# Kernel tuning notes

Measured on AMD Instinct MI355X. Metric: run time of the kernel, lower is better.

Reference implementation:

```python
import jax, jax.numpy as jnp
from jax import lax
import numpy as np

KSIZE = 5  # kernel_size from init
CHANNEL = 256

def _gaussian_kernel2d(sigma, ksize):
    # matches torch: exp(-i^2/(2*sigma^2)) outer product, normalized to sum 1
    n = ksize // 2
    r = jnp.arange(-n, n + 1, dtype=jnp.float32)
    g = jnp.exp(-(r ** 2) / (2.0 * sigma ** 2))
    k2d = g[:, None] * g[None, :]
    return k2d / k2d.sum()

def setup_inputs() -> dict:
    key = jax.random.key(0)
    k1, k2 = jax.random.split(key)
    x = jax.random.normal(k1, (16, CHANNEL, 64, 64), dtype=jnp.float32)
    # sigma is the module's learned scalar; keep away from 0 for a well-defined kernel
    sigma = jax.random.uniform(k2, (1,), dtype=jnp.float32, minval=0.5, maxval=1.5)
    return {"x": x, "sigma": sigma}

def reference(x, sigma):
    # The torch module writes a channel-diagonal weight into a dense Conv2d;
    # mathematically this is a depthwise conv with the same 2D Gaussian per channel.
    C = x.shape[1]
    k2d = _gaussian_kernel2d(sigma[0], KSIZE)
    w = jnp.broadcast_to(k2d[None, None, :, :], (C, 1, KSIZE, KSIZE))  # OIHW, groups=C
    pad = KSIZE // 2
    return lax.conv_general_dilated(
        x, w,
        window_strides=(1, 1),
        padding=[(pad, pad), (pad, pad)],
        dimension_numbers=("NCHW", "OIHW", "NCHW"),
        feature_group_count=C,
    )
```

## Files before the change

kernel.cpp:

```cpp
#include <hip/hip_runtime.h>
#include <math.h>


constexpr int Hh   = 64;
constexpr int Ww   = 64;
constexpr int KS   = 5;
constexpr int PADc = 2;
constexpr int TH   = Hh + 2 * PADc;
constexpr int IN_STR = 72;
constexpr int PPB  = 4;

__global__ __launch_bounds__(256, 4) void gauss5(const float* __restrict__ x,
                                                 const float* __restrict__ sigma,
                                                 float* __restrict__ out) {
    __shared__ alignas(16) float sIn[2][TH * IN_STR];

    const int t = threadIdx.x;
    const size_t plane0 = (size_t)blockIdx.x * PPB;

    const float sg = sigma[0];
    const float c2 = -1.0f / (2.0f * sg * sg);
    float g[KS];
    float gsum = 0.0f;
#pragma unroll
    for (int i = 0; i < KS; ++i) {
        float d = (float)(i - PADc);
        g[i] = expf(d * d * c2);
        gsum += g[i];
    }
    const float ginv = 1.0f / gsum;
#pragma unroll
    for (int i = 0; i < KS; ++i) g[i] *= ginv;

    for (int i = t; i < 528; i += 256) {
        int row, col;
        if (i < 272) {
            int rr = i / 68;
            col = i - rr * 68;
            row = (rr < 2) ? rr : (rr + 64);
        } else {
            int j = i - 272;
            row = 2 + (j >> 2);
            int k = j & 3;
            col = (k < 2) ? k : (k + 64);
        }
        sIn[0][row * IN_STR + col] = 0.0f;
        sIn[1][row * IN_STR + col] = 0.0f;
    }

    const int c4 = t & 15;
    const int r0 = (t >> 4) << 2;

    float4 v[4];
    {
        const float4* __restrict__ x4 = (const float4*)(x + plane0 * (Hh * Ww));
#pragma unroll
        for (int k = 0; k < 4; ++k) v[k] = x4[t + k * 256];
#pragma unroll
        for (int k = 0; k < 4; ++k) {
            int idx = t + k * 256;
            int r   = idx >> 4;
            int c   = (idx & 15) << 2;
            float* dst = &sIn[0][(r + PADc) * IN_STR + c + PADc];
            dst[0] = v[k].x; dst[1] = v[k].y; dst[2] = v[k].z; dst[3] = v[k].w;
        }
    }
    __syncthreads();

    for (int p = 0; p < PPB; ++p) {
        if (p + 1 < PPB) {
            const float4* __restrict__ xn =
                (const float4*)(x + (plane0 + p + 1) * (Hh * Ww));
#pragma unroll
            for (int k = 0; k < 4; ++k) v[k] = xn[t + k * 256];
        }

        const float* __restrict__ buf = sIn[p & 1];
        float4 h[8];
#pragma unroll
        for (int i = 0; i < 8; ++i) {
            const float* src = &buf[(r0 + i) * IN_STR + (c4 << 2)];
            float4 a = *(const float4*)(src);
            float4 b = *(const float4*)(src + 4);
            h[i].x = g[0]*a.x + g[1]*a.y + g[2]*a.z + g[3]*a.w + g[4]*b.x;
            h[i].y = g[0]*a.y + g[1]*a.z + g[2]*a.w + g[3]*b.x + g[4]*b.y;
            h[i].z = g[0]*a.z + g[1]*a.w + g[2]*b.x + g[3]*b.y + g[4]*b.z;
            h[i].w = g[0]*a.w + g[1]*b.x + g[2]*b.y + g[3]*b.z + g[4]*b.w;
        }

        float4* __restrict__ o4 = (float4*)(out + (plane0 + p) * (Hh * Ww));
#pragma unroll
        for (int i = 0; i < 4; ++i) {
            float4 acc;
            acc.x = g[0]*h[i].x; acc.y = g[0]*h[i].y;
            acc.z = g[0]*h[i].z; acc.w = g[0]*h[i].w;
#pragma unroll
            for (int j = 1; j < KS; ++j) {
                acc.x += g[j] * h[i+j].x;
                acc.y += g[j] * h[i+j].y;
                acc.z += g[j] * h[i+j].z;
                acc.w += g[j] * h[i+j].w;
            }
            o4[(r0 + i) * 16 + c4] = acc;
        }

        if (p + 1 < PPB) {
            float* __restrict__ nbuf = sIn[(p + 1) & 1];
#pragma unroll
            for (int k = 0; k < 4; ++k) {
                int idx = t + k * 256;
                int r   = idx >> 4;
                int c   = (idx & 15) << 2;
                float* dst = &nbuf[(r + PADc) * IN_STR + c + PADc];
                dst[0] = v[k].x; dst[1] = v[k].y; dst[2] = v[k].z; dst[3] = v[k].w;
            }
            __syncthreads();
        }
    }
}

extern "C" void kernel_launch(void* const* d_in, const int* in_sizes, int n_in,
                              void* d_out, int out_size, void* d_ws, size_t ws_size,
                              hipStream_t stream) {
    const float* x     = (const float*)d_in[0];
    const float* sigma = (const float*)d_in[1];
    float* out         = (float*)d_out;
    const int planes = in_sizes[0] / (Hh * Ww);
    gauss5<<<planes / PPB, 256, 0, stream>>>(x, sigma, out);
}
```

Baseline: 112.7 us.

## Drop shared-memory staging and read halo directly from global memory per plane

Removes the double-buffered LDS tile and its zero-padded halo. Each thread now loads its 8 input rows straight from global memory, using float4 center loads plus float2 left/right halo loads, and applies masks for the borders. The grid changes from one block per four planes to one block per plane, which gives more blocks and removes the __syncthreads barriers. In exchange, neighbouring threads read overlapping rows redundantly and must rely on L1/L2 to absorb the roughly twofold extra load traffic, and the explicit prefetch overlap is lost.

```diff
diff --git a/kernel.cpp b/kernel.cpp
--- a/kernel.cpp
+++ b/kernel.cpp
@@ -6,17 +6,13 @@
 constexpr int Ww   = 64;
 constexpr int KS   = 5;
 constexpr int PADc = 2;
-constexpr int TH   = Hh + 2 * PADc;
-constexpr int IN_STR = 72;
-constexpr int PPB  = 4;
 
 __global__ __launch_bounds__(256, 4) void gauss5(const float* __restrict__ x,
                                                  const float* __restrict__ sigma,
                                                  float* __restrict__ out) {
-    __shared__ alignas(16) float sIn[2][TH * IN_STR];
-
-    const int t = threadIdx.x;
-    const size_t plane0 = (size_t)blockIdx.x * PPB;
+    const int t  = threadIdx.x;
+    const int c4 = t & 15;
+    const int r0 = (t >> 4) << 2;
 
     const float sg = sigma[0];
     const float c2 = -1.0f / (2.0f * sg * sg);
@@ -32,90 +28,55 @@
 #pragma unroll
     for (int i = 0; i < KS; ++i) g[i] *= ginv;
 
-    for (int i = t; i < 528; i += 256) {
-        int row, col;
-        if (i < 272) {
-            int rr = i / 68;
-            col = i - rr * 68;
-            row = (rr < 2) ? rr : (rr + 64);
-        } else {
-            int j = i - 272;
-            row = 2 + (j >> 2);
-            int k = j & 3;
-            col = (k < 2) ? k : (k + 64);
-        }
-        sIn[0][row * IN_STR + col] = 0.0f;
-        sIn[1][row * IN_STR + col] = 0.0f;
+    const size_t plane = blockIdx.x;
+    const float* __restrict__ xp = x   + plane * (size_t)(Hh * Ww);
+    float* __restrict__ op       = out + plane * (size_t)(Hh * Ww);
+
+    const int   loff  = (c4 > 0)  ? (4 * c4 - 2) : 0;
+    const int   roff  = (c4 < 15) ? (4 * c4 + 4) : 0;
+    const float lmask = (c4 > 0)  ? 1.0f : 0.0f;
+    const float rmask = (c4 < 15) ? 1.0f : 0.0f;
+
+    float4 h[8];
+#pragma unroll
+    for (int i = 0; i < 8; ++i) {
+        const int   rr = r0 - 2 + i;
+        const int   rc = rr < 0 ? 0 : (rr > Hh - 1 ? Hh - 1 : rr);
+        const float rm = (rr >= 0 && rr < Hh) ? 1.0f : 0.0f;
+        const float* row = xp + rc * Ww;
+
+        float4 mv = *(const float4*)(row + 4 * c4);
+        float2 lv = *(const float2*)(row + loff);
+        float2 rv = *(const float2*)(row + roff);
+
+        const float lm  = rm * lmask;
+        const float rm2 = rm * rmask;
+        const float l0 = lv.x * lm,  l1 = lv.y * lm;
+        const float rA = rv.x * rm2, rB = rv.y * rm2;
+        const float m0 = mv.x * rm,  m1 = mv.y * rm;
+        const float m2 = mv.z * rm,  m3 = mv.w * rm;
+
+        h[i].x = g[0]*l0 + g[1]*l1 + g[2]*m0 + g[3]*m1 + g[4]*m2;
+        h[i].y = g[0]*l1 + g[1]*m0 + g[2]*m1 + g[3]*m2 + g[4]*m3;
+        h[i].z = g[0]*m0 + g[1]*m1 + g[2]*m2 + g[3]*m3 + g[4]*rA;
+        h[i].w = g[0]*m1 + g[1]*m2 + g[2]*m3 + g[3]*rA + g[4]*rB;
     }
 
-    const int c4 = t & 15;
-    const int r0 = (t >> 4) << 2;
-
-    float4 v[4];
-    {
-        const float4* __restrict__ x4 = (const float4*)(x + plane0 * (Hh * Ww));
 #pragma unroll
-        for (int k = 0; k < 4; ++k) v[k] = x4[t + k * 256];
+    for (int i = 0; i < 4; ++i) {
+        float4 acc;
+        acc.x = g[0] * h[i].x;
+        acc.y = g[0] * h[i].y;
+        acc.z = g[0] * h[i].z;
+        acc.w = g[0] * h[i].w;
 #pragma unroll
-        for (int k = 0; k < 4; ++k) {
-            int idx = t + k * 256;
-            int r   = idx >> 4;
-            int c   = (idx & 15) << 2;
-            float* dst = &sIn[0][(r + PADc) * IN_STR + c + PADc];
-            dst[0] = v[k].x; dst[1] = v[k].y; dst[2] = v[k].z; dst[3] = v[k].w;
+        for (int j = 1; j < KS; ++j) {
+            acc.x += g[j] * h[i + j].x;
+            acc.y += g[j] * h[i + j].y;
+            acc.z += g[j] * h[i + j].z;
+            acc.w += g[j] * h[i + j].w;
         }
-    }
-    __syncthreads();
-
-    for (int p = 0; p < PPB; ++p) {
-        if (p + 1 < PPB) {
-            const float4* __restrict__ xn =
-                (const float4*)(x + (plane0 + p + 1) * (Hh * Ww));
-#pragma unroll
-            for (int k = 0; k < 4; ++k) v[k] = xn[t + k * 256];
-        }
-
-        const float* __restrict__ buf = sIn[p & 1];
-        float4 h[8];
-#pragma unroll
-        for (int i = 0; i < 8; ++i) {
-            const float* src = &buf[(r0 + i) * IN_STR + (c4 << 2)];
-            float4 a = *(const float4*)(src);
-            float4 b = *(const float4*)(src + 4);
-            h[i].x = g[0]*a.x + g[1]*a.y + g[2]*a.z + g[3]*a.w + g[4]*b.x;
-            h[i].y = g[0]*a.y + g[1]*a.z + g[2]*a.w + g[3]*b.x + g[4]*b.y;
-            h[i].z = g[0]*a.z + g[1]*a.w + g[2]*b.x + g[3]*b.y + g[4]*b.z;
-            h[i].w = g[0]*a.w + g[1]*b.x + g[2]*b.y + g[3]*b.z + g[4]*b.w;
-        }
-
-        float4* __restrict__ o4 = (float4*)(out + (plane0 + p) * (Hh * Ww));
-#pragma unroll
-        for (int i = 0; i < 4; ++i) {
-            float4 acc;
-            acc.x = g[0]*h[i].x; acc.y = g[0]*h[i].y;
-            acc.z = g[0]*h[i].z; acc.w = g[0]*h[i].w;
-#pragma unroll
-            for (int j = 1; j < KS; ++j) {
-                acc.x += g[j] * h[i+j].x;
-                acc.y += g[j] * h[i+j].y;
-                acc.z += g[j] * h[i+j].z;
-                acc.w += g[j] * h[i+j].w;
-            }
-            o4[(r0 + i) * 16 + c4] = acc;
-        }
-
-        if (p + 1 < PPB) {
-            float* __restrict__ nbuf = sIn[(p + 1) & 1];
-#pragma unroll
-            for (int k = 0; k < 4; ++k) {
-                int idx = t + k * 256;
-                int r   = idx >> 4;
-                int c   = (idx & 15) << 2;
-                float* dst = &nbuf[(r + PADc) * IN_STR + c + PADc];
-                dst[0] = v[k].x; dst[1] = v[k].y; dst[2] = v[k].z; dst[3] = v[k].w;
-            }
-            __syncthreads();
-        }
+        *(float4*)(op + (r0 + i) * Ww + 4 * c4) = acc;
     }
 }
 
@@ -126,5 +87,5 @@
     const float* sigma = (const float*)d_in[1];
     float* out         = (float*)d_out;
     const int planes = in_sizes[0] / (Hh * Ww);
-    gauss5<<<planes / PPB, 256, 0, stream>>>(x, sigma, out);
+    gauss5<<<planes, 256, 0, stream>>>(x, sigma, out);
 }
```

New measurement: 121.1 us. +7.5%, slower.
